# Kernel tuning notes

Measured on AMD Instinct MI355X. Metric: run time of the kernel, lower is better.

Reference implementation:

```python
import jax, jax.numpy as jnp
import numpy as np

N_NODES = 100000
TIME_LEN = 128
OUT_CH = 5          # temp_out_dim
KERNEL = 7
STRIDE = 3
CONV_OUT_LEN = (TIME_LEN - KERNEL) // STRIDE + 1  # 41
EMB = 32            # temp_emb_dim
HID = EMB // 2      # 16
N_EDGES = 3200000


def setup_inputs() -> dict:
    key = jax.random.key(0)
    ks = jax.random.split(key, 16)
    x = jax.random.normal(ks[0], (N_NODES, TIME_LEN), dtype=jnp.float32)
    edge_index = jax.random.randint(ks[1], (2, N_EDGES), 0, N_NODES, dtype=jnp.int64)
    s = 0.05
    return {
        "x": x,
        "edge_index": edge_index,
        "conv_w": jax.random.normal(ks[2], (OUT_CH, 1, KERNEL), dtype=jnp.float32) * s,
        "conv_b": jax.random.normal(ks[3], (OUT_CH,), dtype=jnp.float32) * s,
        "fc_w": jax.random.normal(ks[4], (EMB, OUT_CH * CONV_OUT_LEN), dtype=jnp.float32) * s,
        "fc_b": jax.random.normal(ks[5], (EMB,), dtype=jnp.float32) * s,
        "g1w1": jax.random.normal(ks[6], (HID, EMB), dtype=jnp.float32) * s,
        "g1b1": jax.random.normal(ks[7], (HID,), dtype=jnp.float32) * s,
        "g1w2": jax.random.normal(ks[8], (HID, HID), dtype=jnp.float32) * s,
        "g1b2": jax.random.normal(ks[9], (HID,), dtype=jnp.float32) * s,
        "g2w1": jax.random.normal(ks[10], (HID, HID), dtype=jnp.float32) * s,
        "g2b1": jax.random.normal(ks[11], (HID,), dtype=jnp.float32) * s,
        "g2w2": jax.random.normal(ks[12], (HID, HID), dtype=jnp.float32) * s,
        "g2b2": jax.random.normal(ks[13], (HID,), dtype=jnp.float32) * s,
        "ro_w": jax.random.normal(ks[14], (1, HID), dtype=jnp.float32) * s,
        "ro_b": jax.random.normal(ks[15], (1,), dtype=jnp.float32) * s,
    }


def _gin_conv(h, edge_index, w1, b1, w2, b2):
    # sum-aggregate neighbor features into target nodes (eps = 0)
    agg = jax.ops.segment_sum(h[edge_index[0]], edge_index[1], num_segments=N_NODES)
    z = h + agg
    # MLP: Linear -> ReLU -> Linear
    return jax.nn.relu(z @ w1.T + b1) @ w2.T + b2


def reference(x, edge_index, conv_w, conv_b, fc_w, fc_b,
              g1w1, g1b1, g1w2, g1b2, g2w1, g2b1, g2w2, g2b2, ro_w, ro_b):
    n = x.shape[0]
    # temporal Conv1d: [N,1,T] -> [N,OUT_CH,CONV_OUT_LEN]
    h = jax.lax.conv_general_dilated(
        x[:, None, :], conv_w, window_strides=(STRIDE,), padding='VALID',
        dimension_numbers=('NCH', 'OIH', 'NCH'))
    h = jax.nn.relu(h + conv_b[None, :, None])
    h = h.reshape(n, -1)                 # channel-major flatten, matches torch .view
    h = h @ fc_w.T + fc_b                # [N, EMB]
    # GIN layer 1 (+ ReLU between layers)
    h = jax.nn.relu(_gin_conv(h, edge_index, g1w1, g1b1, g1w2, g1b2))
    # GIN layer 2 (no activation after final layer)
    h = _gin_conv(h, edge_index, g2w1, g2b1, g2w2, g2b2)
    return h @ ro_w.T + ro_b             # [N, 1]
```

## Files before the change

kernel.cpp:

```cpp
#include <hip/hip_runtime.h>

#define NN   100000
#define TL   128
#define OC   5
#define KW   7
#define ST   3
#define CL   41
#define FLAT 205
#define EMB  32
#define HID  16
#define NE   3200000

#define BBUCK  391
#define NPB    14336
#define TILE   4096
#define NBIN   782
#define CNODES 64
#define NGB    1563
#define NS     2560
#define SENT   0xFFFFFFFFu

__device__ __forceinline__ void f4add(float4& a, const float4 v) {
    a.x += v.x; a.y += v.y; a.z += v.z; a.w += v.w;
}

__global__ __launch_bounds__(256) void k_prep(
    const float* __restrict__ g1w1, const float* __restrict__ fc_w,
    const float* __restrict__ fc_b,
    float* __restrict__ wcT, float* __restrict__ bc,
    int* __restrict__ gcur)
{
    int tid = threadIdx.x;
    for (int idx = tid; idx < FLAT * HID; idx += 256) {
        int l = idx & 15;
        int j = idx >> 4;
        float s = 0.f;
        #pragma unroll
        for (int m = 0; m < EMB; ++m)
            s = fmaf(g1w1[l * EMB + m], fc_w[m * FLAT + j], s);
        wcT[j * HID + l] = s;
    }
    if (tid < HID) {
        float s = 0.f;
        #pragma unroll
        for (int m = 0; m < EMB; ++m)
            s = fmaf(g1w1[tid * EMB + m], fc_b[m], s);
        bc[tid] = s;
    }
    for (int b = tid; b < BBUCK; b += 256)
        gcur[b] = b * NPB;
}

__global__ __launch_bounds__(256) void k_convfc(
    const float* __restrict__ x,
    const float* __restrict__ conv_w, const float* __restrict__ conv_b,
    const float* __restrict__ wcT,   const float* __restrict__ bc,
    float* __restrict__ p1)
{
    __shared__ float s_x[32 * 129];
    __shared__ float s_h[FLAT * 32];
    const int tid = threadIdx.x;
    const long long n0 = (long long)blockIdx.x * 32;

    const float4* xv = (const float4*)(x + n0 * TL);
    #pragma unroll
    for (int c = 0; c < 4; ++c) {
        int f4  = c * 256 + tid;
        int row = f4 >> 5;
        int c4  = f4 & 31;
        float4 v = xv[f4];
        float* d = s_x + row * 129 + c4 * 4;
        d[0] = v.x; d[1] = v.y; d[2] = v.z; d[3] = v.w;
    }
    __syncthreads();

    for (int idx = tid; idx < FLAT * 32; idx += 256) {
        int n = idx & 31;
        int o = idx >> 5;
        int c = o / CL;
        int t = o - c * CL;
        float acc = conv_b[c];
        const float* wr = conv_w + c * KW;
        const float* xr = s_x + n * 129 + t * ST;
        #pragma unroll
        for (int k = 0; k < KW; ++k)
            acc = fmaf(xr[k], wr[k], acc);
        s_h[o * 32 + n] = fmaxf(acc, 0.f);
    }
    __syncthreads();

    const int l  = tid & 15;
    const int n2 = tid >> 4;
    float a0 = bc[l];
    float a1 = a0;
    #pragma unroll 5
    for (int j = 0; j < FLAT; ++j) {
        float w = wcT[j * HID + l];
        a0 = fmaf(s_h[j * 32 + n2],      w, a0);
        a1 = fmaf(s_h[j * 32 + n2 + 16], w, a1);
    }
    p1[(n0 + n2)      * HID + l] = a0;
    p1[(n0 + n2 + 16) * HID + l] = a1;
}

__global__ __launch_bounds__(256) void k_bin(
    const int* __restrict__ ei, int* __restrict__ gcur,
    unsigned int* __restrict__ gbin)
{
    __shared__ unsigned int s_stage[TILE];
    __shared__ int s_cnt[BBUCK], s_ofs[BBUCK], s_base[BBUCK];
    __shared__ int s_sum[256];

    const int tid = threadIdx.x;
    const int e0  = blockIdx.x * TILE;
    const int cntE = min(TILE, NE - e0);

    for (int b = tid; b < BBUCK; b += 256) s_cnt[b] = 0;
    __syncthreads();

    for (int i = tid; i < cntE; i += 256)
        atomicAdd(&s_cnt[ei[NE + e0 + i] >> 8], 1);
    __syncthreads();

    for (int b = tid; b < BBUCK; b += 256) {
        int c = s_cnt[b];
        s_base[b] = c ? atomicAdd(&gcur[b], (c + 15) & ~15) : 0;
    }

    int v0 = 0, v1 = 0;
    {
        int i0 = tid * 2;
        if (i0     < BBUCK) v0 = s_cnt[i0];
        if (i0 + 1 < BBUCK) v1 = s_cnt[i0 + 1];
    }
    int csum = v0 + v1;
    s_sum[tid] = csum;
    __syncthreads();
    #pragma unroll
    for (int d = 1; d < 256; d <<= 1) {
        int t = (tid >= d) ? s_sum[tid - d] : 0;
        __syncthreads();
        s_sum[tid] += t;
        __syncthreads();
    }
    {
        int run = s_sum[tid] - csum;
        int i0 = tid * 2;
        if (i0     < BBUCK) { s_ofs[i0]     = run; run += v0; }
        if (i0 + 1 < BBUCK) { s_ofs[i0 + 1] = run; }
    }
    __syncthreads();

    for (int i = tid; i < cntE; i += 256) {
        int s = ei[e0 + i];
        int d = ei[NE + e0 + i];
        int b = d >> 8;
        int pos = atomicAdd(&s_ofs[b], 1);
        s_stage[pos] = ((unsigned int)(d & 255) << 17) | (unsigned int)s;
    }
    __syncthreads();

    const int wid = tid >> 6, lane = tid & 63;
    for (int b = wid; b < BBUCK; b += 4) {
        int cnt = s_cnt[b];
        if (!cnt) continue;
        int res = (cnt + 15) & ~15;
        int rdo = s_ofs[b] - cnt;
        int gb  = s_base[b];
        int lim = min(res, b * NPB + NPB - gb);
        for (int j = lane; j < lim; j += 64)
            gbin[(size_t)gb + j] = (j < cnt) ? s_stage[rdo + j] : SENT;
    }
}

__global__ __launch_bounds__(256) void k_sort(
    const unsigned int* __restrict__ gbin, const int* __restrict__ gcur,
    int* __restrict__ goff, int* __restrict__ gsorted)
{
    __shared__ unsigned int s_m[NS];
    __shared__ int s_cnt[CNODES], s_ofs[CNODES], s_loc[CNODES];
    __shared__ int s_n;
    const int tid = threadIdx.x;
    const int b64 = blockIdx.x;
    const int bkt = b64 >> 2, q = b64 & 3;
    const int nslots = min(gcur[bkt] - bkt * NPB, NPB);
    const unsigned int* run = gbin + (size_t)bkt * NPB;

    if (tid < CNODES) s_cnt[tid] = 0;
    if (tid == 0) s_n = 0;
    __syncthreads();

    for (int i = tid; i < nslots; i += 256) {
        unsigned int w = run[i];
        if (w != SENT && (int)(w >> 23) == q) {
            int p = atomicAdd(&s_n, 1);
            if (p < NS) {
                s_m[p] = w;
                atomicAdd(&s_cnt[(w >> 17) & 63], 1);
            }
        }
    }
    __syncthreads();

    if (tid < CNODES) s_ofs[tid] = s_cnt[tid];
    __syncthreads();
    #pragma unroll
    for (int d = 1; d < CNODES; d <<= 1) {
        int t = (tid < CNODES && tid >= d) ? s_ofs[tid - d] : 0;
        __syncthreads();
        if (tid < CNODES) s_ofs[tid] += t;
        __syncthreads();
    }
    if (tid < CNODES) {
        int inc = s_ofs[tid];
        s_loc[tid] = inc - s_cnt[tid];
        goff[(size_t)b64 * 65 + tid + 1] = inc;
    }
    if (tid == 0) goff[(size_t)b64 * 65] = 0;
    __syncthreads();

    const int n = min(s_n, NS);
    int* dst = gsorted + (size_t)b64 * NS;
    for (int i = tid; i < n; i += 256) {
        unsigned int w = s_m[i];
        int pos = atomicAdd(&s_loc[(w >> 17) & 63], 1);
        dst[pos] = (int)(w & 0x1FFFFu);
    }
}

__global__ __launch_bounds__(256) void k_gagg1(
    const float* __restrict__ feat, const int* __restrict__ goff,
    const int* __restrict__ gsorted,
    const float* __restrict__ b1, const float* __restrict__ w2,
    const float* __restrict__ b2, const float* __restrict__ w3,
    float* __restrict__ outfeat)
{
    __shared__ float s_acc[CNODES * 16];
    __shared__ float s_w2[HID * HID], s_w3[HID * HID], s_b1[HID], s_b2[HID];
    __shared__ int s_off[CNODES + 1];
    const int tid = threadIdx.x;
    const int b   = blockIdx.x;

    s_w2[tid] = w2[tid];
    s_w3[tid] = w3[tid];
    if (tid < HID) { s_b1[tid] = b1[tid]; s_b2[tid] = b2[tid]; }
    if (tid < CNODES + 1) s_off[tid] = goff[(size_t)b * 65 + tid];
    __syncthreads();

    const int node = tid >> 2, q = tid & 3;
    const int* srcs = gsorted + (size_t)b * NS;
    const float4* pv = (const float4*)feat;
    float4 acc0 = make_float4(0.f, 0.f, 0.f, 0.f);
    float4 acc1 = make_float4(0.f, 0.f, 0.f, 0.f);
    int j = s_off[node];
    const int e = s_off[node + 1];
    for (; j + 7 < e; j += 8) {
        int s0 = srcs[j],     s1 = srcs[j + 1], s2 = srcs[j + 2], s3 = srcs[j + 3];
        int s4 = srcs[j + 4], s5 = srcs[j + 5], s6 = srcs[j + 6], s7 = srcs[j + 7];
        float4 v0 = pv[(size_t)s0 * 4 + q];
        float4 v1 = pv[(size_t)s1 * 4 + q];
        float4 v2 = pv[(size_t)s2 * 4 + q];
        float4 v3 = pv[(size_t)s3 * 4 + q];
        float4 v4 = pv[(size_t)s4 * 4 + q];
        float4 v5 = pv[(size_t)s5 * 4 + q];
        float4 v6 = pv[(size_t)s6 * 4 + q];
        float4 v7 = pv[(size_t)s7 * 4 + q];
        f4add(acc0, v0); f4add(acc1, v1); f4add(acc0, v2); f4add(acc1, v3);
        f4add(acc0, v4); f4add(acc1, v5); f4add(acc0, v6); f4add(acc1, v7);
    }
    for (; j + 3 < e; j += 4) {
        int s0 = srcs[j], s1 = srcs[j + 1], s2 = srcs[j + 2], s3 = srcs[j + 3];
        float4 v0 = pv[(size_t)s0 * 4 + q];
        float4 v1 = pv[(size_t)s1 * 4 + q];
        float4 v2 = pv[(size_t)s2 * 4 + q];
        float4 v3 = pv[(size_t)s3 * 4 + q];
        f4add(acc0, v0); f4add(acc1, v1); f4add(acc0, v2); f4add(acc1, v3);
    }
    for (; j < e; ++j)
        f4add(acc0, pv[(size_t)srcs[j] * 4 + q]);
    f4add(acc0, acc1);
    ((float4*)s_acc)[node * 4 + q] = acc0;
    __syncthreads();

    const int gn = b * CNODES + tid;
    if (tid < CNODES && gn < NN) {
        const float4* fr = (const float4*)(feat + (size_t)gn * HID);
        const float4* sa = (const float4*)(s_acc + tid * 16);
        float t[HID];
        #pragma unroll
        for (int i2 = 0; i2 < 4; ++i2) {
            float4 f = fr[i2], a = sa[i2];
            t[i2*4+0] = fmaxf(f.x + a.x + s_b1[i2*4+0], 0.f);
            t[i2*4+1] = fmaxf(f.y + a.y + s_b1[i2*4+1], 0.f);
            t[i2*4+2] = fmaxf(f.z + a.z + s_b1[i2*4+2], 0.f);
            t[i2*4+3] = fmaxf(f.w + a.w + s_b1[i2*4+3], 0.f);
        }
        float h[HID];
        #pragma unroll
        for (int i2 = 0; i2 < HID; ++i2) {
            float acc = s_b2[i2];
            #pragma unroll
            for (int jj = 0; jj < HID; ++jj) acc += t[jj] * s_w2[i2 * HID + jj];
            h[i2] = fmaxf(acc, 0.f);
        }
        float o[HID];
        #pragma unroll
        for (int i2 = 0; i2 < HID; ++i2) {
            float acc = 0.f;
            #pragma unroll
            for (int jj = 0; jj < HID; ++jj) acc += h[jj] * s_w3[i2 * HID + jj];
            o[i2] = acc;
        }
        float4* po = (float4*)(outfeat + (size_t)gn * HID);
        #pragma unroll
        for (int i2 = 0; i2 < 4; ++i2)
            po[i2] = make_float4(o[i2*4+0], o[i2*4+1], o[i2*4+2], o[i2*4+3]);
    }
}

__global__ __launch_bounds__(256) void k_gagg2(
    const float* __restrict__ feat, const int* __restrict__ goff,
    const int* __restrict__ gsorted,
    const float* __restrict__ b1, const float* __restrict__ w2,
    const float* __restrict__ b2, const float* __restrict__ row,
    const float* __restrict__ rob,
    float* __restrict__ out)
{
    __shared__ float s_acc[CNODES * 16];
    __shared__ float s_w2[HID * HID], s_b1[HID], s_b2[HID], s_ro[HID];
    __shared__ int s_off[CNODES + 1];
    const int tid = threadIdx.x;
    const int b   = blockIdx.x;

    s_w2[tid] = w2[tid];
    if (tid < HID) { s_b1[tid] = b1[tid]; s_b2[tid] = b2[tid]; s_ro[tid] = row[tid]; }
    if (tid < CNODES + 1) s_off[tid] = goff[(size_t)b * 65 + tid];
    __syncthreads();

    const int node = tid >> 2, q = tid & 3;
    const int* srcs = gsorted + (size_t)b * NS;
    const float4* pv = (const float4*)feat;
    float4 acc0 = make_float4(0.f, 0.f, 0.f, 0.f);
    float4 acc1 = make_float4(0.f, 0.f, 0.f, 0.f);
    int j = s_off[node];
    const int e = s_off[node + 1];
    for (; j + 7 < e; j += 8) {
        int s0 = srcs[j],     s1 = srcs[j + 1], s2 = srcs[j + 2], s3 = srcs[j + 3];
        int s4 = srcs[j + 4], s5 = srcs[j + 5], s6 = srcs[j + 6], s7 = srcs[j + 7];
        float4 v0 = pv[(size_t)s0 * 4 + q];
        float4 v1 = pv[(size_t)s1 * 4 + q];
        float4 v2 = pv[(size_t)s2 * 4 + q];
        float4 v3 = pv[(size_t)s3 * 4 + q];
        float4 v4 = pv[(size_t)s4 * 4 + q];
        float4 v5 = pv[(size_t)s5 * 4 + q];
        float4 v6 = pv[(size_t)s6 * 4 + q];
        float4 v7 = pv[(size_t)s7 * 4 + q];
        f4add(acc0, v0); f4add(acc1, v1); f4add(acc0, v2); f4add(acc1, v3);
        f4add(acc0, v4); f4add(acc1, v5); f4add(acc0, v6); f4add(acc1, v7);
    }
    for (; j + 3 < e; j += 4) {
        int s0 = srcs[j], s1 = srcs[j + 1], s2 = srcs[j + 2], s3 = srcs[j + 3];
        float4 v0 = pv[(size_t)s0 * 4 + q];
        float4 v1 = pv[(size_t)s1 * 4 + q];
        float4 v2 = pv[(size_t)s2 * 4 + q];
        float4 v3 = pv[(size_t)s3 * 4 + q];
        f4add(acc0, v0); f4add(acc1, v1); f4add(acc0, v2); f4add(acc1, v3);
    }
    for (; j < e; ++j)
        f4add(acc0, pv[(size_t)srcs[j] * 4 + q]);
    f4add(acc0, acc1);
    ((float4*)s_acc)[node * 4 + q] = acc0;
    __syncthreads();

    const int gn = b * CNODES + tid;
    if (tid < CNODES && gn < NN) {
        const float4* fr = (const float4*)(feat + (size_t)gn * HID);
        const float4* sa = (const float4*)(s_acc + tid * 16);
        float t[HID];
        #pragma unroll
        for (int i2 = 0; i2 < 4; ++i2) {
            float4 f = fr[i2], a = sa[i2];
            t[i2*4+0] = fmaxf(f.x + a.x + s_b1[i2*4+0], 0.f);
            t[i2*4+1] = fmaxf(f.y + a.y + s_b1[i2*4+1], 0.f);
            t[i2*4+2] = fmaxf(f.z + a.z + s_b1[i2*4+2], 0.f);
            t[i2*4+3] = fmaxf(f.w + a.w + s_b1[i2*4+3], 0.f);
        }
        float res = rob[0];
        #pragma unroll
        for (int i2 = 0; i2 < HID; ++i2) {
            float acc = s_b2[i2];
            #pragma unroll
            for (int jj = 0; jj < HID; ++jj) acc += t[jj] * s_w2[i2 * HID + jj];
            res += acc * s_ro[i2];
        }
        out[gn] = res;
    }
}

__global__ __launch_bounds__(256) void k_embed(
    const float* __restrict__ x,
    const float* __restrict__ conv_w, const float* __restrict__ conv_b,
    const float* __restrict__ fc_w,   const float* __restrict__ fc_b,
    const float* __restrict__ g1w1,
    float* __restrict__ p1)
{
    __shared__ float s_x[4][TL];
    __shared__ float s_h[4][FLAT + 3];
    __shared__ float s_e[4][EMB];

    const int w    = threadIdx.x >> 6;
    const int lane = threadIdx.x & 63;
    const int node = blockIdx.x * 4 + w;

    const float2* xr = (const float2*)(x + (size_t)node * TL);
    float2 v = xr[lane];
    s_x[w][lane * 2 + 0] = v.x;
    s_x[w][lane * 2 + 1] = v.y;
    __syncthreads();

    for (int o = lane; o < FLAT; o += 64) {
        int c = o / CL;
        int t = o - c * CL;
        float acc = conv_b[c];
        #pragma unroll
        for (int k = 0; k < KW; ++k)
            acc += s_x[w][t * ST + k] * conv_w[c * KW + k];
        s_h[w][o] = fmaxf(acc, 0.f);
    }
    __syncthreads();

    if (lane < EMB) {
        float acc = fc_b[lane];
        const float* wr = fc_w + lane * FLAT;
        for (int j = 0; j < FLAT; ++j)
            acc += s_h[w][j] * wr[j];
        s_e[w][lane] = acc;
    }
    __syncthreads();

    if (lane < HID) {
        float acc = 0.f;
        const float* wr = g1w1 + lane * EMB;
        #pragma unroll
        for (int j = 0; j < EMB; ++j)
            acc += s_e[w][j] * wr[j];
        p1[(size_t)node * HID + lane] = acc;
    }
}

__global__ __launch_bounds__(256) void k_scatter(
    const float* __restrict__ p, const int* __restrict__ ei,
    float* __restrict__ agg)
{
    long long t = (long long)blockIdx.x * 256 + threadIdx.x;
    int e = (int)(t >> 4);
    int k = (int)(t & 15);
    if (e >= NE) return;
    int src = ei[e];
    int dst = ei[NE + e];
    float v = p[(size_t)src * HID + k];
    atomicAdd(agg + (size_t)dst * HID + k, v);
}

__global__ __launch_bounds__(256) void k_mlp1(
    const float* __restrict__ p1, const float* __restrict__ agg,
    const float* __restrict__ b1, const float* __restrict__ w2,
    const float* __restrict__ b2, const float* __restrict__ w3,
    float* __restrict__ p2)
{
    __shared__ float s_w2[HID * HID], s_w3[HID * HID], s_b1[HID], s_b2[HID];
    int tid = threadIdx.x;
    s_w2[tid] = w2[tid];
    s_w3[tid] = w3[tid];
    if (tid < HID) { s_b1[tid] = b1[tid]; s_b2[tid] = b2[tid]; }
    __syncthreads();

    int n = blockIdx.x * 256 + tid;
    if (n >= NN) return;

    float t[HID], h[HID];
    const float4* pa = (const float4*)(p1  + (size_t)n * HID);
    const float4* pb = (const float4*)(agg + (size_t)n * HID);
    #pragma unroll
    for (int i = 0; i < 4; ++i) {
        float4 a = pa[i], b = pb[i];
        t[i*4+0] = fmaxf(a.x + b.x + s_b1[i*4+0], 0.f);
        t[i*4+1] = fmaxf(a.y + b.y + s_b1[i*4+1], 0.f);
        t[i*4+2] = fmaxf(a.z + b.z + s_b1[i*4+2], 0.f);
        t[i*4+3] = fmaxf(a.w + b.w + s_b1[i*4+3], 0.f);
    }
    #pragma unroll
    for (int i = 0; i < HID; ++i) {
        float acc = s_b2[i];
        #pragma unroll
        for (int j = 0; j < HID; ++j) acc += t[j] * s_w2[i * HID + j];
        h[i] = fmaxf(acc, 0.f);
    }
    float o[HID];
    #pragma unroll
    for (int i = 0; i < HID; ++i) {
        float acc = 0.f;
        #pragma unroll
        for (int j = 0; j < HID; ++j) acc += h[j] * s_w3[i * HID + j];
        o[i] = acc;
    }
    float4* po = (float4*)(p2 + (size_t)n * HID);
    #pragma unroll
    for (int i = 0; i < 4; ++i)
        po[i] = make_float4(o[i*4+0], o[i*4+1], o[i*4+2], o[i*4+3]);
}

__global__ __launch_bounds__(256) void k_final(
    const float* __restrict__ p2, const float* __restrict__ agg2,
    const float* __restrict__ b1, const float* __restrict__ w2,
    const float* __restrict__ b2, const float* __restrict__ row,
    const float* __restrict__ rob,
    float* __restrict__ out)
{
    __shared__ float s_w2[HID * HID], s_b1[HID], s_b2[HID], s_ro[HID];
    int tid = threadIdx.x;
    s_w2[tid] = w2[tid];
    if (tid < HID) { s_b1[tid] = b1[tid]; s_b2[tid] = b2[tid]; s_ro[tid] = row[tid]; }
    __syncthreads();

    int n = blockIdx.x * 256 + tid;
    if (n >= NN) return;

    float t[HID];
    const float4* pa = (const float4*)(p2   + (size_t)n * HID);
    const float4* pb = (const float4*)(agg2 + (size_t)n * HID);
    #pragma unroll
    for (int i = 0; i < 4; ++i) {
        float4 a = pa[i], b = pb[i];
        t[i*4+0] = fmaxf(a.x + b.x + s_b1[i*4+0], 0.f);
        t[i*4+1] = fmaxf(a.y + b.y + s_b1[i*4+1], 0.f);
        t[i*4+2] = fmaxf(a.z + b.z + s_b1[i*4+2], 0.f);
        t[i*4+3] = fmaxf(a.w + b.w + s_b1[i*4+3], 0.f);
    }
    float res = rob[0];
    #pragma unroll
    for (int i = 0; i < HID; ++i) {
        float acc = s_b2[i];
        #pragma unroll
        for (int j = 0; j < HID; ++j) acc += t[j] * s_w2[i * HID + j];
        res += acc * s_ro[i];
    }
    out[n] = res;
}

extern "C" void kernel_launch(void* const* d_in, const int* in_sizes, int n_in,
                              void* d_out, int out_size, void* d_ws, size_t ws_size,
                              hipStream_t stream)
{
    const float* x      = (const float*)d_in[0];
    const int*   ei     = (const int*)  d_in[1];
    const float* conv_w = (const float*)d_in[2];
    const float* conv_b = (const float*)d_in[3];
    const float* fc_w   = (const float*)d_in[4];
    const float* fc_b   = (const float*)d_in[5];
    const float* g1w1   = (const float*)d_in[6];
    const float* g1b1   = (const float*)d_in[7];
    const float* g1w2   = (const float*)d_in[8];
    const float* g1b2   = (const float*)d_in[9];
    const float* g2w1   = (const float*)d_in[10];
    const float* g2b1   = (const float*)d_in[11];
    const float* g2w2   = (const float*)d_in[12];
    const float* g2b2   = (const float*)d_in[13];
    const float* ro_w   = (const float*)d_in[14];
    const float* ro_b   = (const float*)d_in[15];
    float* out = (float*)d_out;

    float* A    = (float*)d_ws;
    float* B    = A + (size_t)NN * HID;
    float* wcT  = B + (size_t)NN * HID;
    float* bc   = wcT + (size_t)FLAT * HID;
    int*   gcur = (int*)(bc + 16);
    unsigned int* gbin = (unsigned int*)(gcur + BBUCK);
    int*   goff    = (int*)(gbin + (size_t)BBUCK * NPB);
    int*   gsorted = goff + (size_t)NGB * 65;
    const size_t need = (size_t)((char*)(gsorted + (size_t)NGB * NS) - (char*)d_ws);

    if (ws_size >= need) {
        k_prep<<<1, 256, 0, stream>>>(g1w1, fc_w, fc_b, wcT, bc, gcur);
        k_convfc<<<NN / 32, 256, 0, stream>>>(x, conv_w, conv_b, wcT, bc, A);
        k_bin<<<NBIN, 256, 0, stream>>>(ei, gcur, gbin);
        k_sort<<<NGB, 256, 0, stream>>>(gbin, gcur, goff, gsorted);
        k_gagg1<<<NGB, 256, 0, stream>>>(A, goff, gsorted, g1b1, g1w2, g1b2,
                                         g2w1, B);
        k_gagg2<<<NGB, 256, 0, stream>>>(B, goff, gsorted, g2b1, g2w2, g2b2,
                                         ro_w, ro_b, out);
    } else {
        k_embed<<<NN / 4, 256, 0, stream>>>(x, conv_w, conv_b, fc_w, fc_b,
                                            g1w1, A);
        hipMemsetAsync(B, 0, (size_t)NN * HID * sizeof(float), stream);
        k_scatter<<<(int)(((long long)NE * HID) / 256), 256, 0, stream>>>(A, ei, B);
        k_mlp1<<<(NN + 255) / 256, 256, 0, stream>>>(A, B, g1b1, g1w2, g1b2,
                                                     g2w1, A);
        hipMemsetAsync(B, 0, (size_t)NN * HID * sizeof(float), stream);
        k_scatter<<<(int)(((long long)NE * HID) / 256), 256, 0, stream>>>(A, ei, B);
        k_final<<<(NN + 255) / 256, 256, 0, stream>>>(A, B, g2b1, g2w2, g2b2,
                                                      ro_w, ro_b, out);
    }
}
```

Baseline: 367.3 us.

## Pad conv output per node and vectorize conv and fused-FC loops with float4

Changes the intermediate conv activation layout from channel-major across nodes to node-major rows padded to 44 per channel, and the folded FC/GIN weight to a matching padded per-output layout. Each conv thread now computes four adjacent outputs from 16 register-cached inputs and writes a float4, while the FC loop reads weights and activations as float4. The aim is fewer LDS instructions and scalar global weight loads in k_convfc. The cost is larger shared memory, which may lower occupancy, and possible LDS bank conflicts from the 220-float row stride.

```diff
diff --git a/kernel.cpp b/kernel.cpp
--- a/kernel.cpp
+++ b/kernel.cpp
@@ -11,6 +11,10 @@
 #define HID  16
 #define NE   3200000
 
+#define CLP  44
+#define JP   220
+#define JB   55
+
 #define BBUCK  391
 #define NPB    14336
 #define TILE   4096
@@ -27,18 +31,23 @@
 __global__ __launch_bounds__(256) void k_prep(
     const float* __restrict__ g1w1, const float* __restrict__ fc_w,
     const float* __restrict__ fc_b,
-    float* __restrict__ wcT, float* __restrict__ bc,
+    float* __restrict__ wcTl, float* __restrict__ bc,
     int* __restrict__ gcur)
 {
     int tid = threadIdx.x;
-    for (int idx = tid; idx < FLAT * HID; idx += 256) {
-        int l = idx & 15;
-        int j = idx >> 4;
+    for (int idx = tid; idx < HID * JP; idx += 256) {
+        int l  = idx / JP;
+        int jp = idx - l * JP;
+        int c  = jp / CLP;
+        int t  = jp - c * CLP;
         float s = 0.f;
-        #pragma unroll
-        for (int m = 0; m < EMB; ++m)
-            s = fmaf(g1w1[l * EMB + m], fc_w[m * FLAT + j], s);
-        wcT[j * HID + l] = s;
+        if (t < CL) {
+            int j = c * CL + t;
+            #pragma unroll
+            for (int m = 0; m < EMB; ++m)
+                s = fmaf(g1w1[l * EMB + m], fc_w[m * FLAT + j], s);
+        }
+        wcTl[idx] = s;
     }
     if (tid < HID) {
         float s = 0.f;
@@ -54,11 +63,11 @@
 __global__ __launch_bounds__(256) void k_convfc(
     const float* __restrict__ x,
     const float* __restrict__ conv_w, const float* __restrict__ conv_b,
-    const float* __restrict__ wcT,   const float* __restrict__ bc,
+    const float* __restrict__ wcTl,  const float* __restrict__ bc,
     float* __restrict__ p1)
 {
-    __shared__ float s_x[32 * 129];
-    __shared__ float s_h[FLAT * 32];
+    __shared__ float s_x[32 * 129 + 8];
+    __shared__ float s_h2[32 * JP];
     const int tid = threadIdx.x;
     const long long n0 = (long long)blockIdx.x * 32;
 
@@ -74,18 +83,33 @@
     }
     __syncthreads();
 
-    for (int idx = tid; idx < FLAT * 32; idx += 256) {
-        int n = idx & 31;
-        int o = idx >> 5;
-        int c = o / CL;
-        int t = o - c * CL;
-        float acc = conv_b[c];
+    for (int i = tid; i < 55 * 32; i += 256) {
+        int n  = i & 31;
+        int ci = i >> 5;
+        int c  = ci / 11;
+        int tg = ci - c * 11;
+        int t0 = tg * 4;
+        const float* xr = s_x + n * 129 + t0 * ST;
+        float xx[16];
+        #pragma unroll
+        for (int k = 0; k < 16; ++k) xx[k] = xr[k];
         const float* wr = conv_w + c * KW;
-        const float* xr = s_x + n * 129 + t * ST;
-        #pragma unroll
-        for (int k = 0; k < KW; ++k)
-            acc = fmaf(xr[k], wr[k], acc);
-        s_h[o * 32 + n] = fmaxf(acc, 0.f);
+        float w0 = wr[0], w1 = wr[1], w2 = wr[2], w3 = wr[3],
+              w4 = wr[4], w5 = wr[5], w6 = wr[6];
+        float bb = conv_b[c];
+        float4 r;
+        r.x = fmaxf(bb + xx[0]*w0 + xx[1]*w1 + xx[2]*w2 + xx[3]*w3
+                       + xx[4]*w4 + xx[5]*w5 + xx[6]*w6, 0.f);
+        r.y = (t0 + 1 < CL)
+            ? fmaxf(bb + xx[3]*w0 + xx[4]*w1 + xx[5]*w2 + xx[6]*w3
+                       + xx[7]*w4 + xx[8]*w5 + xx[9]*w6, 0.f) : 0.f;
+        r.z = (t0 + 2 < CL)
+            ? fmaxf(bb + xx[6]*w0 + xx[7]*w1 + xx[8]*w2 + xx[9]*w3
+                       + xx[10]*w4 + xx[11]*w5 + xx[12]*w6, 0.f) : 0.f;
+        r.w = (t0 + 3 < CL)
+            ? fmaxf(bb + xx[9]*w0 + xx[10]*w1 + xx[11]*w2 + xx[12]*w3
+                       + xx[13]*w4 + xx[14]*w5 + xx[15]*w6, 0.f) : 0.f;
+        *(float4*)(s_h2 + n * JP + c * CLP + t0) = r;
     }
     __syncthreads();
 
@@ -93,11 +117,16 @@
     const int n2 = tid >> 4;
     float a0 = bc[l];
     float a1 = a0;
+    const float4* wl = (const float4*)(wcTl + l * JP);
+    const float4* h0 = (const float4*)(s_h2 + n2 * JP);
+    const float4* h1 = (const float4*)(s_h2 + (n2 + 16) * JP);
     #pragma unroll 5
-    for (int j = 0; j < FLAT; ++j) {
-        float w = wcT[j * HID + l];
-        a0 = fmaf(s_h[j * 32 + n2],      w, a0);
-        a1 = fmaf(s_h[j * 32 + n2 + 16], w, a1);
+    for (int jb = 0; jb < JB; ++jb) {
+        float4 w = wl[jb];
+        float4 p = h0[jb];
+        float4 q = h1[jb];
+        a0 = fmaf(p.x, w.x, fmaf(p.y, w.y, fmaf(p.z, w.z, fmaf(p.w, w.w, a0))));
+        a1 = fmaf(q.x, w.x, fmaf(q.y, w.y, fmaf(q.z, w.z, fmaf(q.w, w.w, a1))));
     }
     p1[(n0 + n2)      * HID + l] = a0;
     p1[(n0 + n2 + 16) * HID + l] = a1;
@@ -572,8 +601,8 @@
 
     float* A    = (float*)d_ws;
     float* B    = A + (size_t)NN * HID;
-    float* wcT  = B + (size_t)NN * HID;
-    float* bc   = wcT + (size_t)FLAT * HID;
+    float* wcTl = B + (size_t)NN * HID;
+    float* bc   = wcTl + (size_t)HID * JP;
     int*   gcur = (int*)(bc + 16);
     unsigned int* gbin = (unsigned int*)(gcur + BBUCK);
     int*   goff    = (int*)(gbin + (size_t)BBUCK * NPB);
@@ -581,8 +610,8 @@
     const size_t need = (size_t)((char*)(gsorted + (size_t)NGB * NS) - (char*)d_ws);
 
     if (ws_size >= need) {
-        k_prep<<<1, 256, 0, stream>>>(g1w1, fc_w, fc_b, wcT, bc, gcur);
-        k_convfc<<<NN / 32, 256, 0, stream>>>(x, conv_w, conv_b, wcT, bc, A);
+        k_prep<<<1, 256, 0, stream>>>(g1w1, fc_w, fc_b, wcTl, bc, gcur);
+        k_convfc<<<NN / 32, 256, 0, stream>>>(x, conv_w, conv_b, wcTl, bc, A);
         k_bin<<<NBIN, 256, 0, stream>>>(ei, gcur, gbin);
         k_sort<<<NGB, 256, 0, stream>>>(gbin, gcur, goff, gsorted);
         k_gagg1<<<NGB, 256, 0, stream>>>(A, goff, gsorted, g1b1, g1w2, g1b2,
```

Result: faster. 360.0 us (-2.0%).

## Restructure conv+FC kernel into per-wave fused compute with shuffle reduction

Applied to the files above, without the earlier changes.

The conv+FC embedding kernel is rewritten so each wavefront handles 8 nodes, with 8 lanes per node splitting the 205 flattened conv outputs. Each lane computes conv outputs on the fly and accumulates all 16 outputs using float4 weight loads, then reduces across lanes with shuffles. This removes the shared s_h buffer and the block-wide barriers, and cuts LDS use so more blocks can be resident (launch bounds now request 6). The weight matrix is padded to 208 rows with zeros so the strided loop stays uniform. The barrier is replaced by an lgkmcnt wait, which relies on each wave reading only its own LDS slice.

```diff
diff --git a/kernel.cpp b/kernel.cpp
--- a/kernel.cpp
+++ b/kernel.cpp
@@ -11,6 +11,9 @@
 #define HID  16
 #define NE   3200000
 
+#define JPAD 208
+#define SXW  1032
+
 #define BBUCK  391
 #define NPB    14336
 #define TILE   4096
@@ -27,18 +30,20 @@
 __global__ __launch_bounds__(256) void k_prep(
     const float* __restrict__ g1w1, const float* __restrict__ fc_w,
     const float* __restrict__ fc_b,
-    float* __restrict__ wcT, float* __restrict__ bc,
+    float* __restrict__ wcTj, float* __restrict__ bc,
     int* __restrict__ gcur)
 {
     int tid = threadIdx.x;
-    for (int idx = tid; idx < FLAT * HID; idx += 256) {
+    for (int idx = tid; idx < JPAD * HID; idx += 256) {
+        int j = idx >> 4;
         int l = idx & 15;
-        int j = idx >> 4;
         float s = 0.f;
-        #pragma unroll
-        for (int m = 0; m < EMB; ++m)
-            s = fmaf(g1w1[l * EMB + m], fc_w[m * FLAT + j], s);
-        wcT[j * HID + l] = s;
+        if (j < FLAT) {
+            #pragma unroll
+            for (int m = 0; m < EMB; ++m)
+                s = fmaf(g1w1[l * EMB + m], fc_w[m * FLAT + j], s);
+        }
+        wcTj[idx] = s;
     }
     if (tid < HID) {
         float s = 0.f;
@@ -51,56 +56,93 @@
         gcur[b] = b * NPB;
 }
 
-__global__ __launch_bounds__(256) void k_convfc(
+__global__ __launch_bounds__(256, 6) void k_convfc(
     const float* __restrict__ x,
     const float* __restrict__ conv_w, const float* __restrict__ conv_b,
-    const float* __restrict__ wcT,   const float* __restrict__ bc,
+    const float* __restrict__ wcTj,  const float* __restrict__ bc,
     float* __restrict__ p1)
 {
-    __shared__ float s_x[32 * 129];
-    __shared__ float s_h[FLAT * 32];
-    const int tid = threadIdx.x;
-    const long long n0 = (long long)blockIdx.x * 32;
-
-    const float4* xv = (const float4*)(x + n0 * TL);
-    #pragma unroll
-    for (int c = 0; c < 4; ++c) {
-        int f4  = c * 256 + tid;
+    __shared__ float s_x[4 * SXW];
+    const int tid  = threadIdx.x;
+    const int wv   = tid >> 6;
+    const int lane = tid & 63;
+    const int n    = lane >> 3;
+    const int g    = lane & 7;
+    const long long nw = (long long)blockIdx.x * 32 + wv * 8;
+
+    float* sx = s_x + wv * SXW;
+
+    const float4* xv = (const float4*)(x + nw * TL);
+    #pragma unroll
+    for (int cc = 0; cc < 4; ++cc) {
+        int f4  = cc * 64 + lane;
         int row = f4 >> 5;
         int c4  = f4 & 31;
         float4 v = xv[f4];
-        float* d = s_x + row * 129 + c4 * 4;
+        float* d = sx + row * 129 + c4 * 4;
         d[0] = v.x; d[1] = v.y; d[2] = v.z; d[3] = v.w;
     }
-    __syncthreads();
-
-    for (int idx = tid; idx < FLAT * 32; idx += 256) {
-        int n = idx & 31;
-        int o = idx >> 5;
-        int c = o / CL;
-        int t = o - c * CL;
-        float acc = conv_b[c];
-        const float* wr = conv_w + c * KW;
-        const float* xr = s_x + n * 129 + t * ST;
-        #pragma unroll
-        for (int k = 0; k < KW; ++k)
-            acc = fmaf(xr[k], wr[k], acc);
-        s_h[o * 32 + n] = fmaxf(acc, 0.f);
-    }
-    __syncthreads();
-
-    const int l  = tid & 15;
-    const int n2 = tid >> 4;
-    float a0 = bc[l];
-    float a1 = a0;
-    #pragma unroll 5
-    for (int j = 0; j < FLAT; ++j) {
-        float w = wcT[j * HID + l];
-        a0 = fmaf(s_h[j * 32 + n2],      w, a0);
-        a1 = fmaf(s_h[j * 32 + n2 + 16], w, a1);
-    }
-    p1[(n0 + n2)      * HID + l] = a0;
-    p1[(n0 + n2 + 16) * HID + l] = a1;
+    asm volatile("s_waitcnt lgkmcnt(0)" ::: "memory");
+
+    float acc[16];
+    #pragma unroll
+    for (int l = 0; l < 16; ++l) acc[l] = 0.f;
+
+    const float* xrow = sx + n * 129;
+    const float4* wp = (const float4*)(wcTj) + g * 4;
+    int t = g, c = 0;
+    #pragma unroll 2
+    for (int jj = 0; jj < 26; ++jj) {
+        if (c < OC) {
+            const float* xr = xrow + t * ST;
+            const float* cw = conv_w + c * KW;
+            float h = conv_b[c];
+            #pragma unroll
+            for (int k = 0; k < KW; ++k) h = fmaf(xr[k], cw[k], h);
+            h = fmaxf(h, 0.f);
+            float4 w0 = wp[0], w1 = wp[1], w2 = wp[2], w3 = wp[3];
+            acc[0]  = fmaf(h, w0.x, acc[0]);
+            acc[1]  = fmaf(h, w0.y, acc[1]);
+            acc[2]  = fmaf(h, w0.z, acc[2]);
+            acc[3]  = fmaf(h, w0.w, acc[3]);
+            acc[4]  = fmaf(h, w1.x, acc[4]);
+            acc[5]  = fmaf(h, w1.y, acc[5]);
+            acc[6]  = fmaf(h, w1.z, acc[6]);
+            acc[7]  = fmaf(h, w1.w, acc[7]);
+            acc[8]  = fmaf(h, w2.x, acc[8]);
+            acc[9]  = fmaf(h, w2.y, acc[9]);
+            acc[10] = fmaf(h, w2.z, acc[10]);
+            acc[11] = fmaf(h, w2.w, acc[11]);
+            acc[12] = fmaf(h, w3.x, acc[12]);
+            acc[13] = fmaf(h, w3.y, acc[13]);
+            acc[14] = fmaf(h, w3.z, acc[14]);
+            acc[15] = fmaf(h, w3.w, acc[15]);
+        }
+        t += 8;
+        if (t >= CL) { t -= CL; ++c; }
+        wp += 32;
+    }
+
+    #pragma unroll
+    for (int l = 0; l < 16; ++l) {
+        acc[l] += __shfl_xor(acc[l], 1);
+        acc[l] += __shfl_xor(acc[l], 2);
+        acc[l] += __shfl_xor(acc[l], 4);
+    }
+
+    if (g == 0) {
+        const float4* bcv = (const float4*)bc;
+        float4 b0 = bcv[0], b1 = bcv[1], b2 = bcv[2], b3 = bcv[3];
+        float4* po = (float4*)(p1 + (nw + n) * HID);
+        po[0] = make_float4(acc[0]  + b0.x, acc[1]  + b0.y,
+                            acc[2]  + b0.z, acc[3]  + b0.w);
+        po[1] = make_float4(acc[4]  + b1.x, acc[5]  + b1.y,
+                            acc[6]  + b1.z, acc[7]  + b1.w);
+        po[2] = make_float4(acc[8]  + b2.x, acc[9]  + b2.y,
+                            acc[10] + b2.z, acc[11] + b2.w);
+        po[3] = make_float4(acc[12] + b3.x, acc[13] + b3.y,
+                            acc[14] + b3.z, acc[15] + b3.w);
+    }
 }
 
 __global__ __launch_bounds__(256) void k_bin(
@@ -572,8 +614,8 @@
 
     float* A    = (float*)d_ws;
     float* B    = A + (size_t)NN * HID;
-    float* wcT  = B + (size_t)NN * HID;
-    float* bc   = wcT + (size_t)FLAT * HID;
+    float* wcTj = B + (size_t)NN * HID;
+    float* bc   = wcTj + (size_t)JPAD * HID;
     int*   gcur = (int*)(bc + 16);
     unsigned int* gbin = (unsigned int*)(gcur + BBUCK);
     int*   goff    = (int*)(gbin + (size_t)BBUCK * NPB);
@@ -581,8 +623,8 @@
     const size_t need = (size_t)((char*)(gsorted + (size_t)NGB * NS) - (char*)d_ws);
 
     if (ws_size >= need) {
-        k_prep<<<1, 256, 0, stream>>>(g1w1, fc_w, fc_b, wcT, bc, gcur);
-        k_convfc<<<NN / 32, 256, 0, stream>>>(x, conv_w, conv_b, wcT, bc, A);
+        k_prep<<<1, 256, 0, stream>>>(g1w1, fc_w, fc_b, wcTj, bc, gcur);
+        k_convfc<<<NN / 32, 256, 0, stream>>>(x, conv_w, conv_b, wcTj, bc, A);
         k_bin<<<NBIN, 256, 0, stream>>>(ei, gcur, gbin);
         k_sort<<<NGB, 256, 0, stream>>>(gbin, gcur, goff, gsorted);
         k_gagg1<<<NGB, 256, 0, stream>>>(A, goff, gsorted, g1b1, g1w2, g1b2,
```

New measurement: 403.2 us. 9.8% more time.
